# Kernel optimization log

Measured on AMD Instinct MI355X. Metric: run time of the kernel, lower is better.

Reference implementation:

```python
import jax, jax.numpy as jnp
import numpy as np

E = 512      # embed_dim
H = 8        # num_heads
HD = E // H  # head_dim
TGT = 512
SRC = 2048
B = 16


def setup_inputs() -> dict:
    key = jax.random.key(0)
    ks = jax.random.split(key, 10)
    inp = {
        "query": jax.random.normal(ks[0], (TGT, B, E), dtype=jnp.float32),
        "key": jax.random.normal(ks[1], (SRC, B, E), dtype=jnp.float32),
        "value": jax.random.normal(ks[2], (SRC, B, E), dtype=jnp.float32),
        "in_proj_weight": jax.random.normal(ks[3], (3 * E, E), dtype=jnp.float32) * 0.02,
        "in_proj_bias": jax.random.normal(ks[4], (3 * E,), dtype=jnp.float32) * 0.02,
        "bias_k": jax.random.normal(ks[5], (1, 1, E), dtype=jnp.float32) * 0.02,
        "bias_v": jax.random.normal(ks[6], (1, 1, E), dtype=jnp.float32) * 0.02,
        "out_proj_weight": jax.random.normal(ks[7], (E, E), dtype=jnp.float32) * 0.02,
        "out_proj_bias": jnp.zeros((E,), dtype=jnp.float32),
        "key_padding_mask": jax.random.randint(ks[8], (B, SRC), 0, 2).astype(bool),
    }
    return inp


def reference(query, key, value, in_proj_weight, in_proj_bias, bias_k, bias_v,
              out_proj_weight, out_proj_bias, key_padding_mask):
    tgt_len, bsz, embed_dim = query.shape
    scaling = float(HD) ** -0.5

    # manual in-projection (query != key, key is value -> separate q, fused kv)
    q = query @ in_proj_weight[:E].T + in_proj_bias[:E]
    k = key @ in_proj_weight[E:2 * E].T + in_proj_bias[E:2 * E]
    v = value @ in_proj_weight[2 * E:].T + in_proj_bias[2 * E:]
    q = q * scaling

    # bias_k / bias_v concatenation along src dim; pad key_padding_mask with False
    k = jnp.concatenate([k, jnp.broadcast_to(bias_k, (1, bsz, E))], axis=0)
    v = jnp.concatenate([v, jnp.broadcast_to(bias_v, (1, bsz, E))], axis=0)
    kpm = jnp.pad(key_padding_mask, ((0, 0), (0, 1)))  # [B, SRC+1]

    src_len = k.shape[0]
    # [len, B, E] -> [B*H, len, HD]
    q = q.reshape(tgt_len, bsz * H, HD).transpose(1, 0, 2)
    k = k.reshape(src_len, bsz * H, HD).transpose(1, 0, 2)
    v = v.reshape(src_len, bsz * H, HD).transpose(1, 0, 2)

    scores = jnp.einsum('bth,bsh->bts', q, k)  # [B*H, TGT, SRC+1]
    mask = kpm[:, None, None, :]               # [B, 1, 1, SRC+1]
    scores = scores.reshape(bsz, H, tgt_len, src_len)
    scores = jnp.where(mask, -jnp.inf, scores).reshape(bsz * H, tgt_len, src_len)
    attn = jax.nn.softmax(scores, axis=-1)

    out = jnp.einsum('bts,bsh->bth', attn, v)                 # [B*H, TGT, HD]
    out = out.transpose(1, 0, 2).reshape(tgt_len, bsz, E)     # [TGT, B, E]
    out = out @ out_proj_weight.T + out_proj_bias
    return out, attn
```

## Files before the change

kernel.cpp:

```cpp
#include <hip/hip_runtime.h>

#define E    512
#define H    8
#define HD   64
#define TGT  512
#define SRC  2048
#define S1   2049
#define S1P  2112
#define NB   16
#define BH   128
#define NCH  33

typedef __attribute__((ext_vector_type(8))) short short8;
typedef __attribute__((ext_vector_type(4))) float floatx4;

__device__ __forceinline__ unsigned short f2bf(float x) {
    unsigned u = __float_as_uint(x);
    u = (u + 0x7FFF + ((u >> 16) & 1)) >> 16;
    return (unsigned short)u;
}

__global__ __launch_bounds__(256) void cvt_bf16(const float* __restrict__ src,
    unsigned short* __restrict__ dst, const int n8)
{
    const int i = blockIdx.x * 256 + threadIdx.x;
    if (i >= n8) return;
    const float4 f0 = ((const float4*)src)[(size_t)i * 2];
    const float4 f1 = ((const float4*)src)[(size_t)i * 2 + 1];
    unsigned short o[8] = {f2bf(f0.x), f2bf(f0.y), f2bf(f0.z), f2bf(f0.w),
                           f2bf(f1.x), f2bf(f1.y), f2bf(f1.z), f2bf(f1.w)};
    ((int4*)dst)[i] = *(int4*)o;
}

__global__ __launch_bounds__(256) void proj_gemm(const unsigned short* __restrict__ X,
    const unsigned short* __restrict__ W, const float* __restrict__ bias,
    unsigned short* __restrict__ Y, const int ld, const float scale)
{
    __shared__ __align__(16) unsigned short As[128][72];
    __shared__ __align__(16) unsigned short Bs[64][72];
    const int tid  = threadIdx.x;
    const int c0   = blockIdx.x << 6;
    const int r0   = blockIdx.y << 7;
    const int w    = tid >> 6, lane = tid & 63, c = lane & 15, quad = lane >> 4;
    floatx4 acc[2][4] = {};
    for (int k0 = 0; k0 < E; k0 += 64) {
#pragma unroll
        for (int i = 0; i < 4; ++i) {
            const int idx = tid + (i << 8);
            const int r = idx >> 3, q = (idx & 7) << 3;
            *(int4*)&As[r][q] = *(const int4*)&X[(size_t)(r0 + r) * E + k0 + q];
        }
#pragma unroll
        for (int i = 0; i < 2; ++i) {
            const int idx = tid + (i << 8);
            const int r = idx >> 3, q = (idx & 7) << 3;
            *(int4*)&Bs[r][q] = *(const int4*)&W[(size_t)(c0 + r) * E + k0 + q];
        }
        __syncthreads();
#pragma unroll
        for (int kh = 0; kh < 2; ++kh) {
            short8 a0 = *(const short8*)&As[(w << 5) + c][(kh << 5) + (quad << 3)];
            short8 a1 = *(const short8*)&As[(w << 5) + 16 + c][(kh << 5) + (quad << 3)];
#pragma unroll
            for (int n = 0; n < 4; ++n) {
                short8 b = *(const short8*)&Bs[(n << 4) + c][(kh << 5) + (quad << 3)];
                acc[0][n] = __builtin_amdgcn_mfma_f32_16x16x32_bf16(a0, b, acc[0][n], 0, 0, 0);
                acc[1][n] = __builtin_amdgcn_mfma_f32_16x16x32_bf16(a1, b, acc[1][n], 0, 0, 0);
            }
        }
        __syncthreads();
    }
#pragma unroll
    for (int mt = 0; mt < 2; ++mt) {
#pragma unroll
        for (int reg = 0; reg < 4; ++reg) {
            const int rg = r0 + (w << 5) + (mt << 4) + (quad << 2) + reg;
            const int t = rg >> 4, b = rg & 15;
#pragma unroll
            for (int n = 0; n < 4; ++n) {
                const int col = c0 + (n << 4) + c;
                const int h = col >> 6, hd = col & 63;
                const float v = (acc[mt][n][reg] + bias[col]) * scale;
                Y[((size_t)(b * H + h) * ld + t) * HD + hd] = f2bf(v);
            }
        }
    }
}

__global__ void fill_bias(const float* __restrict__ bk, const float* __restrict__ bv,
                          unsigned short* __restrict__ kbuf, unsigned short* __restrict__ vtbuf)
{
    const int idx = blockIdx.x * 256 + threadIdx.x;
    const int bh = idx >> 6, hd = idx & 63, h = bh & 7;
    kbuf[((size_t)bh * S1P + SRC) * HD + hd] = f2bf(bk[h * HD + hd]);
    vtbuf[((size_t)bh * HD + hd) * S1P + SRC] = f2bf(bv[h * HD + hd]);
}

__global__ __launch_bounds__(256) void transpose_v(const unsigned short* __restrict__ vbuf,
    unsigned short* __restrict__ vtbuf)
{
    __shared__ __align__(16) unsigned short T[64][72];
    const int tid = threadIdx.x;
    const int s0  = blockIdx.x << 6;
    const int bh  = blockIdx.y;
#pragma unroll
    for (int i = 0; i < 2; ++i) {
        const int idx = tid + (i << 8);
        const int s = idx >> 3, q = (idx & 7) << 3;
        *(int4*)&T[s][q] = *(const int4*)&vbuf[((size_t)bh * SRC + s0 + s) * HD + q];
    }
    __syncthreads();
#pragma unroll
    for (int i = 0; i < 2; ++i) {
        const int idx = tid + (i << 8);
        const int hd = idx >> 3, sq = (idx & 7) << 3;
        unsigned short tmp[8];
#pragma unroll
        for (int j = 0; j < 8; ++j) tmp[j] = T[sq + j][hd];
        *(int4*)&vtbuf[((size_t)bh * HD + hd) * S1P + s0 + sq] = *(int4*)tmp;
    }
}

__global__ __launch_bounds__(256) void stats_kernel(const unsigned short* __restrict__ qbh,
    const unsigned short* __restrict__ kbuf, const int* __restrict__ kpm,
    float* __restrict__ lsum)
{
    __shared__ __align__(16) unsigned short Qs[64][72];
    __shared__ __align__(16) unsigned short Ks[64][72];
    __shared__ float mf[64];
    const int tid = threadIdx.x;
    const int t0  = blockIdx.x << 6;
    const int bh  = blockIdx.y;
    const int bb  = bh >> 3;
    const int w   = tid >> 6, lane = tid & 63, c = lane & 15, quad = lane >> 4;
#pragma unroll
    for (int i = 0; i < 2; ++i) {
        const int idx = tid + (i << 8);
        const int r = idx >> 3, q = (idx & 7) << 3;
        *(int4*)&Qs[r][q] = *(const int4*)&qbh[((size_t)bh * TGT + t0 + r) * HD + q];
    }
    float rs[4] = {0.f, 0.f, 0.f, 0.f};
    for (int ch = 0; ch < NCH; ++ch) {
        const int s0 = ch << 6;
#pragma unroll
        for (int i = 0; i < 2; ++i) {
            const int idx = tid + (i << 8);
            const int r = idx >> 3, q = (idx & 7) << 3;
            *(int4*)&Ks[r][q] = *(const int4*)&kbuf[((size_t)bh * S1P + s0 + r) * HD + q];
        }
        if (tid < 64) {
            const int s = s0 + tid;
            mf[tid] = (s < SRC) ? (kpm[bb * SRC + s] ? 3e38f : 0.f)
                                : ((s == SRC) ? 0.f : 3e38f);
        }
        __syncthreads();
        floatx4 sc[4] = {};
#pragma unroll
        for (int kh = 0; kh < 2; ++kh) {
            short8 a = *(const short8*)&Qs[(w << 4) + c][(kh << 5) + (quad << 3)];
#pragma unroll
            for (int n = 0; n < 4; ++n) {
                short8 b = *(const short8*)&Ks[(n << 4) + c][(kh << 5) + (quad << 3)];
                sc[n] = __builtin_amdgcn_mfma_f32_16x16x32_bf16(a, b, sc[n], 0, 0, 0);
            }
        }
#pragma unroll
        for (int n = 0; n < 4; ++n) {
            const float m = mf[(n << 4) + c];
#pragma unroll
            for (int reg = 0; reg < 4; ++reg)
                rs[reg] += __expf(sc[n][reg] - m);
        }
        __syncthreads();
    }
#pragma unroll
    for (int reg = 0; reg < 4; ++reg) {
        float v = rs[reg];
        v += __shfl_xor(v, 1); v += __shfl_xor(v, 2);
        v += __shfl_xor(v, 4); v += __shfl_xor(v, 8);
        rs[reg] = v;
    }
    if (c == 0) {
        const int t = t0 + (w << 4) + (quad << 2);
#pragma unroll
        for (int reg = 0; reg < 4; ++reg)
            lsum[bh * TGT + t + reg] = rs[reg];
    }
}

__global__ __launch_bounds__(256) void attn_pv(const unsigned short* __restrict__ qbh,
    const unsigned short* __restrict__ kbuf, const unsigned short* __restrict__ vtbuf,
    const int* __restrict__ kpm, const float* __restrict__ lsum,
    float* __restrict__ attn, unsigned short* __restrict__ ctx)
{
    __shared__ __align__(16) unsigned short Qs[64][72];
    __shared__ __align__(16) unsigned short Ks[64][72];
    __shared__ __align__(16) unsigned short Vs[64][72];
    __shared__ __align__(16) unsigned short Ps[4][16][72];
    __shared__ float linv[64];
    __shared__ float mf[64];
    const int tid = threadIdx.x;
    const int t0  = blockIdx.x << 6;
    const int bh  = blockIdx.y;
    const int bb  = bh >> 3;
    const int w   = tid >> 6, lane = tid & 63, c = lane & 15, quad = lane >> 4;
#pragma unroll
    for (int i = 0; i < 2; ++i) {
        const int idx = tid + (i << 8);
        const int r = idx >> 3, q = (idx & 7) << 3;
        *(int4*)&Qs[r][q] = *(const int4*)&qbh[((size_t)bh * TGT + t0 + r) * HD + q];
    }
    if (tid < 64) linv[tid] = 1.0f / lsum[bh * TGT + t0 + tid];
    __syncthreads();
    float li[4];
#pragma unroll
    for (int reg = 0; reg < 4; ++reg) li[reg] = linv[(w << 4) + (quad << 2) + reg];
    const size_t arow = ((size_t)bh * TGT + t0 + (w << 4) + (quad << 2)) * S1;
    floatx4 ca[4] = {};
    for (int ch = 0; ch < NCH; ++ch) {
        const int s0 = ch << 6;
#pragma unroll
        for (int i = 0; i < 2; ++i) {
            const int idx = tid + (i << 8);
            const int r = idx >> 3, q = (idx & 7) << 3;
            *(int4*)&Ks[r][q] = *(const int4*)&kbuf[((size_t)bh * S1P + s0 + r) * HD + q];
            *(int4*)&Vs[r][q] = *(const int4*)&vtbuf[((size_t)bh * HD + r) * S1P + s0 + q];
        }
        if (tid < 64) {
            const int s = s0 + tid;
            mf[tid] = (s < SRC) ? (kpm[bb * SRC + s] ? 3e38f : 0.f)
                                : ((s == SRC) ? 0.f : 3e38f);
        }
        __syncthreads();
        floatx4 sc[4] = {};
#pragma unroll
        for (int kh = 0; kh < 2; ++kh) {
            short8 a = *(const short8*)&Qs[(w << 4) + c][(kh << 5) + (quad << 3)];
#pragma unroll
            for (int n = 0; n < 4; ++n) {
                short8 b = *(const short8*)&Ks[(n << 4) + c][(kh << 5) + (quad << 3)];
                sc[n] = __builtin_amdgcn_mfma_f32_16x16x32_bf16(a, b, sc[n], 0, 0, 0);
            }
        }
#pragma unroll
        for (int n = 0; n < 4; ++n) {
            const float m = mf[(n << 4) + c];
            const int s = s0 + (n << 4) + c;
#pragma unroll
            for (int reg = 0; reg < 4; ++reg) {
                const float p = __expf(sc[n][reg] - m) * li[reg];
                if (s < S1) attn[arow + (size_t)reg * S1 + s] = p;
                Ps[w][(quad << 2) + reg][(n << 4) + c] = f2bf(p);
            }
        }
        __syncthreads();
#pragma unroll
        for (int kh = 0; kh < 2; ++kh) {
            short8 a = *(const short8*)&Ps[w][c][(kh << 5) + (quad << 3)];
#pragma unroll
            for (int n = 0; n < 4; ++n) {
                short8 b = *(const short8*)&Vs[(n << 4) + c][(kh << 5) + (quad << 3)];
                ca[n] = __builtin_amdgcn_mfma_f32_16x16x32_bf16(a, b, ca[n], 0, 0, 0);
            }
        }
        __syncthreads();
    }
#pragma unroll
    for (int reg = 0; reg < 4; ++reg) {
        const int t = t0 + (w << 4) + (quad << 2) + reg;
#pragma unroll
        for (int n = 0; n < 4; ++n)
            ctx[((size_t)bh * TGT + t) * HD + (n << 4) + c] = f2bf(ca[n][reg]);
    }
}

__global__ __launch_bounds__(256) void outproj_gemm(const unsigned short* __restrict__ ctx,
    const unsigned short* __restrict__ W, const float* __restrict__ bias,
    float* __restrict__ out)
{
    __shared__ __align__(16) unsigned short As[128][72];
    __shared__ __align__(16) unsigned short Bs[64][72];
    const int tid = threadIdx.x;
    const int c0  = blockIdx.x << 6;
    const int r0  = blockIdx.y << 7;
    const int w   = tid >> 6, lane = tid & 63, c = lane & 15, quad = lane >> 4;
    floatx4 acc[2][4] = {};
    for (int k0 = 0; k0 < E; k0 += 64) {
        const int h = k0 >> 6;
#pragma unroll
        for (int i = 0; i < 4; ++i) {
            const int idx = tid + (i << 8);
            const int r = idx >> 3, q = (idx & 7) << 3;
            const int rg = r0 + r, t = rg >> 4, b = rg & 15;
            *(int4*)&As[r][q] = *(const int4*)&ctx[((size_t)(b * H + h) * TGT + t) * HD + q];
        }
#pragma unroll
        for (int i = 0; i < 2; ++i) {
            const int idx = tid + (i << 8);
            const int r = idx >> 3, q = (idx & 7) << 3;
            *(int4*)&Bs[r][q] = *(const int4*)&W[(size_t)(c0 + r) * E + k0 + q];
        }
        __syncthreads();
#pragma unroll
        for (int kh = 0; kh < 2; ++kh) {
            short8 a0 = *(const short8*)&As[(w << 5) + c][(kh << 5) + (quad << 3)];
            short8 a1 = *(const short8*)&As[(w << 5) + 16 + c][(kh << 5) + (quad << 3)];
#pragma unroll
            for (int n = 0; n < 4; ++n) {
                short8 b = *(const short8*)&Bs[(n << 4) + c][(kh << 5) + (quad << 3)];
                acc[0][n] = __builtin_amdgcn_mfma_f32_16x16x32_bf16(a0, b, acc[0][n], 0, 0, 0);
                acc[1][n] = __builtin_amdgcn_mfma_f32_16x16x32_bf16(a1, b, acc[1][n], 0, 0, 0);
            }
        }
        __syncthreads();
    }
#pragma unroll
    for (int mt = 0; mt < 2; ++mt) {
#pragma unroll
        for (int reg = 0; reg < 4; ++reg) {
            const int rg = r0 + (w << 5) + (mt << 4) + (quad << 2) + reg;
#pragma unroll
            for (int n = 0; n < 4; ++n) {
                const int col = c0 + (n << 4) + c;
                out[(size_t)rg * E + col] = acc[mt][n][reg] + bias[col];
            }
        }
    }
}

extern "C" void kernel_launch(void* const* d_in, const int* in_sizes, int n_in,
                              void* d_out, int out_size, void* d_ws, size_t ws_size,
                              hipStream_t stream)
{
    const float* query  = (const float*)d_in[0];
    const float* key    = (const float*)d_in[1];
    const float* value  = (const float*)d_in[2];
    const float* ipw    = (const float*)d_in[3];
    const float* ipb    = (const float*)d_in[4];
    const float* bias_k = (const float*)d_in[5];
    const float* bias_v = (const float*)d_in[6];
    const float* opw    = (const float*)d_in[7];
    const float* opb    = (const float*)d_in[8];
    const int*   kpm    = (const int*)d_in[9];

    float* out  = (float*)d_out;
    float* attn = out + (size_t)TGT * NB * E;

    unsigned short* k_bf = (unsigned short*)attn;
    unsigned short* v_bf = k_bf + (size_t)16777216;
    unsigned short* vbuf = v_bf + (size_t)16777216;

    char* ws = (char*)d_ws;
    unsigned short* q_bf  = (unsigned short*)ws;
    unsigned short* wi_bf = q_bf  + (size_t)4194304;
    unsigned short* wo_bf = wi_bf + (size_t)786432;
    unsigned short* qbh   = wo_bf + (size_t)262144;
    unsigned short* kbuf  = qbh   + (size_t)4194304;
    unsigned short* vtbuf = kbuf  + (size_t)17301504;
    unsigned short* ctx   = vtbuf + (size_t)17301504;
    float*          lsum  = (float*)(ctx + (size_t)4194304);

    cvt_bf16<<<dim3(2048), 256, 0, stream>>>(query, q_bf, 524288);
    cvt_bf16<<<dim3(8192), 256, 0, stream>>>(key,   k_bf, 2097152);
    cvt_bf16<<<dim3(8192), 256, 0, stream>>>(value, v_bf, 2097152);
    cvt_bf16<<<dim3(384),  256, 0, stream>>>(ipw,   wi_bf, 98304);
    cvt_bf16<<<dim3(128),  256, 0, stream>>>(opw,   wo_bf, 32768);

    proj_gemm<<<dim3(8, 64),  256, 0, stream>>>(q_bf, wi_bf,          ipb,         qbh,  TGT, 0.125f);
    proj_gemm<<<dim3(8, 256), 256, 0, stream>>>(k_bf, wi_bf + 262144, ipb + E,     kbuf, S1P, 1.0f);
    proj_gemm<<<dim3(8, 256), 256, 0, stream>>>(v_bf, wi_bf + 524288, ipb + 2 * E, vbuf, SRC, 1.0f);

    fill_bias<<<dim3(32), 256, 0, stream>>>(bias_k, bias_v, kbuf, vtbuf);
    transpose_v<<<dim3(32, 128), 256, 0, stream>>>(vbuf, vtbuf);

    stats_kernel<<<dim3(8, 128), 256, 0, stream>>>(qbh, kbuf, kpm, lsum);
    attn_pv<<<dim3(8, 128), 256, 0, stream>>>(qbh, kbuf, vtbuf, kpm, lsum, attn, ctx);
    outproj_gemm<<<dim3(8, 64), 256, 0, stream>>>(ctx, wo_bf, opb, out);
}
```

Baseline: 1.097 ms.

## Fuse softmax stats and PV into single kernel keeping full P row in LDS

```diff
diff --git a/kernel.cpp b/kernel.cpp
--- a/kernel.cpp
+++ b/kernel.cpp
@@ -10,6 +10,7 @@
 #define NB   16
 #define BH   128
 #define NCH  33
+#define PW   2120
 
 typedef __attribute__((ext_vector_type(8))) short short8;
 typedef __attribute__((ext_vector_type(4))) float floatx4;
@@ -94,6 +95,10 @@
     const int bh = idx >> 6, hd = idx & 63, h = bh & 7;
     kbuf[((size_t)bh * S1P + SRC) * HD + hd] = f2bf(bk[h * HD + hd]);
     vtbuf[((size_t)bh * HD + hd) * S1P + SRC] = f2bf(bv[h * HD + hd]);
+    for (int s = SRC + 1; s < S1P; ++s) {
+        kbuf[((size_t)bh * S1P + s) * HD + hd] = 0;
+        vtbuf[((size_t)bh * HD + hd) * S1P + s] = 0;
+    }
 }
 
 __global__ __launch_bounds__(256) void transpose_v(const unsigned short* __restrict__ vbuf,
@@ -121,58 +126,58 @@
     }
 }
 
-__global__ __launch_bounds__(256) void stats_kernel(const unsigned short* __restrict__ qbh,
-    const unsigned short* __restrict__ kbuf, const int* __restrict__ kpm,
-    float* __restrict__ lsum)
-{
-    __shared__ __align__(16) unsigned short Qs[64][72];
-    __shared__ __align__(16) unsigned short Ks[64][72];
-    __shared__ float mf[64];
+__global__ __launch_bounds__(256, 2) void attn_fused(
+    const unsigned short* __restrict__ qbh,
+    const unsigned short* __restrict__ kbuf,
+    const unsigned short* __restrict__ vtbuf,
+    const int* __restrict__ kpm,
+    float* __restrict__ attn, unsigned short* __restrict__ ctx)
+{
+    __shared__ __align__(16) unsigned short P[16][PW];
+    __shared__ float mf[S1P];
+    __shared__ float sums[4][16];
+    __shared__ float linv[16];
     const int tid = threadIdx.x;
-    const int t0  = blockIdx.x << 6;
+    const int t0  = blockIdx.x << 4;
     const int bh  = blockIdx.y;
     const int bb  = bh >> 3;
-    const int w   = tid >> 6, lane = tid & 63, c = lane & 15, quad = lane >> 4;
-#pragma unroll
-    for (int i = 0; i < 2; ++i) {
-        const int idx = tid + (i << 8);
-        const int r = idx >> 3, q = (idx & 7) << 3;
-        *(int4*)&Qs[r][q] = *(const int4*)&qbh[((size_t)bh * TGT + t0 + r) * HD + q];
-    }
+    const int w = tid >> 6, lane = tid & 63, c = lane & 15, quad = lane >> 4;
+
+    for (int s = tid; s < S1P; s += 256)
+        mf[s] = (s < SRC) ? (kpm[bb * SRC + s] ? 3e38f : 0.f)
+                          : ((s == SRC) ? 0.f : 3e38f);
+
+    const unsigned short* qr = &qbh[((size_t)bh * TGT + t0 + c) * HD + (quad << 3)];
+    short8 qa0 = *(const short8*)qr;
+    short8 qa1 = *(const short8*)(qr + 32);
+
+    __syncthreads();
+
     float rs[4] = {0.f, 0.f, 0.f, 0.f};
-    for (int ch = 0; ch < NCH; ++ch) {
+    for (int ch = w; ch < NCH; ch += 4) {
         const int s0 = ch << 6;
-#pragma unroll
-        for (int i = 0; i < 2; ++i) {
-            const int idx = tid + (i << 8);
-            const int r = idx >> 3, q = (idx & 7) << 3;
-            *(int4*)&Ks[r][q] = *(const int4*)&kbuf[((size_t)bh * S1P + s0 + r) * HD + q];
-        }
-        if (tid < 64) {
-            const int s = s0 + tid;
-            mf[tid] = (s < SRC) ? (kpm[bb * SRC + s] ? 3e38f : 0.f)
-                                : ((s == SRC) ? 0.f : 3e38f);
-        }
-        __syncthreads();
         floatx4 sc[4] = {};
 #pragma unroll
-        for (int kh = 0; kh < 2; ++kh) {
-            short8 a = *(const short8*)&Qs[(w << 4) + c][(kh << 5) + (quad << 3)];
-#pragma unroll
-            for (int n = 0; n < 4; ++n) {
-                short8 b = *(const short8*)&Ks[(n << 4) + c][(kh << 5) + (quad << 3)];
-                sc[n] = __builtin_amdgcn_mfma_f32_16x16x32_bf16(a, b, sc[n], 0, 0, 0);
-            }
-        }
-#pragma unroll
         for (int n = 0; n < 4; ++n) {
-            const float m = mf[(n << 4) + c];
-#pragma unroll
-            for (int reg = 0; reg < 4; ++reg)
-                rs[reg] += __expf(sc[n][reg] - m);
-        }
-        __syncthreads();
-    }
+            const unsigned short* kr =
+                &kbuf[((size_t)bh * S1P + s0 + (n << 4) + c) * HD + (quad << 3)];
+            short8 b0 = *(const short8*)kr;
+            short8 b1 = *(const short8*)(kr + 32);
+            sc[n] = __builtin_amdgcn_mfma_f32_16x16x32_bf16(qa0, b0, sc[n], 0, 0, 0);
+            sc[n] = __builtin_amdgcn_mfma_f32_16x16x32_bf16(qa1, b1, sc[n], 0, 0, 0);
+        }
+#pragma unroll
+        for (int n = 0; n < 4; ++n) {
+            const float m = mf[s0 + (n << 4) + c];
+#pragma unroll
+            for (int reg = 0; reg < 4; ++reg) {
+                const float p = __expf(sc[n][reg] - m);
+                rs[reg] += p;
+                P[(quad << 2) + reg][s0 + (n << 4) + c] = f2bf(p);
+            }
+        }
+    }
+
 #pragma unroll
     for (int reg = 0; reg < 4; ++reg) {
         float v = rs[reg];
@@ -181,96 +186,44 @@
         rs[reg] = v;
     }
     if (c == 0) {
-        const int t = t0 + (w << 4) + (quad << 2);
 #pragma unroll
         for (int reg = 0; reg < 4; ++reg)
-            lsum[bh * TGT + t + reg] = rs[reg];
-    }
-}
-
-__global__ __launch_bounds__(256) void attn_pv(const unsigned short* __restrict__ qbh,
-    const unsigned short* __restrict__ kbuf, const unsigned short* __restrict__ vtbuf,
-    const int* __restrict__ kpm, const float* __restrict__ lsum,
-    float* __restrict__ attn, unsigned short* __restrict__ ctx)
-{
-    __shared__ __align__(16) unsigned short Qs[64][72];
-    __shared__ __align__(16) unsigned short Ks[64][72];
-    __shared__ __align__(16) unsigned short Vs[64][72];
-    __shared__ __align__(16) unsigned short Ps[4][16][72];
-    __shared__ float linv[64];
-    __shared__ float mf[64];
-    const int tid = threadIdx.x;
-    const int t0  = blockIdx.x << 6;
-    const int bh  = blockIdx.y;
-    const int bb  = bh >> 3;
-    const int w   = tid >> 6, lane = tid & 63, c = lane & 15, quad = lane >> 4;
-#pragma unroll
-    for (int i = 0; i < 2; ++i) {
-        const int idx = tid + (i << 8);
-        const int r = idx >> 3, q = (idx & 7) << 3;
-        *(int4*)&Qs[r][q] = *(const int4*)&qbh[((size_t)bh * TGT + t0 + r) * HD + q];
-    }
-    if (tid < 64) linv[tid] = 1.0f / lsum[bh * TGT + t0 + tid];
+            sums[w][(quad << 2) + reg] = rs[reg];
+    }
     __syncthreads();
-    float li[4];
-#pragma unroll
-    for (int reg = 0; reg < 4; ++reg) li[reg] = linv[(w << 4) + (quad << 2) + reg];
-    const size_t arow = ((size_t)bh * TGT + t0 + (w << 4) + (quad << 2)) * S1;
-    floatx4 ca[4] = {};
-    for (int ch = 0; ch < NCH; ++ch) {
+    if (tid < 16)
+        linv[tid] = 1.0f / (sums[0][tid] + sums[1][tid] + sums[2][tid] + sums[3][tid]);
+    __syncthreads();
+
+    floatx4 ca = {};
+#pragma unroll 6
+    for (int kc = 0; kc < 66; ++kc) {
+        short8 a = *(const short8*)&P[c][(kc << 5) + (quad << 3)];
+        short8 b = *(const short8*)&vtbuf[((size_t)bh * HD + (w << 4) + c) * S1P
+                                          + (kc << 5) + (quad << 3)];
+        ca = __builtin_amdgcn_mfma_f32_16x16x32_bf16(a, b, ca, 0, 0, 0);
+    }
+#pragma unroll
+    for (int reg = 0; reg < 4; ++reg) {
+        const int t = t0 + (quad << 2) + reg;
+        ctx[((size_t)bh * TGT + t) * HD + (w << 4) + c] =
+            f2bf(ca[reg] * linv[(quad << 2) + reg]);
+    }
+
+    for (int ch = w; ch < NCH; ch += 4) {
         const int s0 = ch << 6;
-#pragma unroll
-        for (int i = 0; i < 2; ++i) {
-            const int idx = tid + (i << 8);
-            const int r = idx >> 3, q = (idx & 7) << 3;
-            *(int4*)&Ks[r][q] = *(const int4*)&kbuf[((size_t)bh * S1P + s0 + r) * HD + q];
-            *(int4*)&Vs[r][q] = *(const int4*)&vtbuf[((size_t)bh * HD + r) * S1P + s0 + q];
-        }
-        if (tid < 64) {
-            const int s = s0 + tid;
-            mf[tid] = (s < SRC) ? (kpm[bb * SRC + s] ? 3e38f : 0.f)
-                                : ((s == SRC) ? 0.f : 3e38f);
-        }
-        __syncthreads();
-        floatx4 sc[4] = {};
-#pragma unroll
-        for (int kh = 0; kh < 2; ++kh) {
-            short8 a = *(const short8*)&Qs[(w << 4) + c][(kh << 5) + (quad << 3)];
-#pragma unroll
-            for (int n = 0; n < 4; ++n) {
-                short8 b = *(const short8*)&Ks[(n << 4) + c][(kh << 5) + (quad << 3)];
-                sc[n] = __builtin_amdgcn_mfma_f32_16x16x32_bf16(a, b, sc[n], 0, 0, 0);
-            }
-        }
-#pragma unroll
-        for (int n = 0; n < 4; ++n) {
-            const float m = mf[(n << 4) + c];
-            const int s = s0 + (n << 4) + c;
-#pragma unroll
-            for (int reg = 0; reg < 4; ++reg) {
-                const float p = __expf(sc[n][reg] - m) * li[reg];
-                if (s < S1) attn[arow + (size_t)reg * S1 + s] = p;
-                Ps[w][(quad << 2) + reg][(n << 4) + c] = f2bf(p);
-            }
-        }
-        __syncthreads();
-#pragma unroll
-        for (int kh = 0; kh < 2; ++kh) {
-            short8 a = *(const short8*)&Ps[w][c][(kh << 5) + (quad << 3)];
-#pragma unroll
-            for (int n = 0; n < 4; ++n) {
-                short8 b = *(const short8*)&Vs[(n << 4) + c][(kh << 5) + (quad << 3)];
-                ca[n] = __builtin_amdgcn_mfma_f32_16x16x32_bf16(a, b, ca[n], 0, 0, 0);
-            }
-        }
-        __syncthreads();
-    }
-#pragma unroll
-    for (int reg = 0; reg < 4; ++reg) {
-        const int t = t0 + (w << 4) + (quad << 2) + reg;
-#pragma unroll
-        for (int n = 0; n < 4; ++n)
-            ctx[((size_t)bh * TGT + t) * HD + (n << 4) + c] = f2bf(ca[n][reg]);
+        if (ch < 32) {
+#pragma unroll
+            for (int r = 0; r < 16; ++r) {
+                const float p =
+                    __uint_as_float((unsigned)P[r][s0 + lane] << 16) * linv[r];
+                attn[((size_t)bh * TGT + t0 + r) * S1 + s0 + lane] = p;
+            }
+        } else if (lane < 16) {
+            const float p =
+                __uint_as_float((unsigned)P[lane][2048] << 16) * linv[lane];
+            attn[((size_t)bh * TGT + t0 + lane) * S1 + 2048] = p;
+        }
     }
 }
 
@@ -358,7 +311,6 @@
     unsigned short* kbuf  = qbh   + (size_t)4194304;
     unsigned short* vtbuf = kbuf  + (size_t)17301504;
     unsigned short* ctx   = vtbuf + (size_t)17301504;
-    float*          lsum  = (float*)(ctx + (size_t)4194304);
 
     cvt_bf16<<<dim3(2048), 256, 0, stream>>>(query, q_bf, 524288);
     cvt_bf16<<<dim3(8192), 256, 0, stream>>>(key,   k_bf, 2097152);
@@ -373,7 +325,6 @@
     fill_bias<<<dim3(32), 256, 0, stream>>>(bias_k, bias_v, kbuf, vtbuf);
     transpose_v<<<dim3(32, 128), 256, 0, stream>>>(vbuf, vtbuf);
 
-    stats_kernel<<<dim3(8, 128), 256, 0, stream>>>(qbh, kbuf, kpm, lsum);
-    attn_pv<<<dim3(8, 128), 256, 0, stream>>>(qbh, kbuf, vtbuf, kpm, lsum, attn, ctx);
+    attn_fused<<<dim3(32, 128), 256, 0, stream>>>(qbh, kbuf, vtbuf, kpm, attn, ctx);
     outproj_gemm<<<dim3(8, 64), 256, 0, stream>>>(ctx, wo_bf, opb, out);
 }
```

Measured after the change: 1.106 ms. Within noise of the previous version (+0.9%).
